# Optimization experiments

Hardware: AMD Instinct MI355X
Metric: run time of the kernel (lower is better)

The kernel has to match this reference:

```python
import jax, jax.numpy as jnp
import numpy as np

EPS = 1e-5


def _gcn_conv(x, src, dst, n_nodes, W, b):
    # x: [N, Fin]; src/dst: [E+N] (self-loops already appended)
    h = x @ W                                   # [N, Fout]
    deg = jnp.zeros((n_nodes,), x.dtype).at[dst].add(1.0)
    dinv = jax.lax.rsqrt(deg)                   # deg >= 1 due to self-loops
    norm = dinv[src] * dinv[dst]                # [E+N]
    msg = h[src] * norm[:, None]                # [E+N, Fout]  (gather)
    out = jax.ops.segment_sum(msg, dst, num_segments=n_nodes)  # scatter-add
    return out + b


def _bn_relu(x, gamma, beta):
    # BatchNorm over nodes (training-style batch statistics), then ReLU.
    mu = jnp.mean(x, axis=0)
    var = jnp.mean((x - mu) ** 2, axis=0)       # biased variance (torch BN)
    xn = (x - mu) * jax.lax.rsqrt(var + EPS)
    return jax.nn.relu(xn * gamma + beta)


def setup_inputs() -> dict:
    key = jax.random.key(0)
    ks = jax.random.split(key, 12)
    N, E, Fin, H, O, G = 100000, 1600000, 128, 128, 64, 128
    x = jax.random.normal(ks[0], (N, Fin), dtype=jnp.float32)
    edge_index = jax.random.randint(ks[1], (2, E), 0, N, dtype=jnp.int64)
    batch = jnp.sort(jax.random.randint(ks[2], (N,), 0, G, dtype=jnp.int64))
    s = 1.0 / np.sqrt(Fin)
    W0 = jax.random.uniform(ks[3], (Fin, H), jnp.float32, -s, s)
    b0 = jnp.zeros((H,), jnp.float32)
    g0 = jnp.ones((H,), jnp.float32)
    be0 = jnp.zeros((H,), jnp.float32)
    s2 = 1.0 / np.sqrt(H)
    W1 = jax.random.uniform(ks[4], (H, H), jnp.float32, -s2, s2)
    b1 = jnp.zeros((H,), jnp.float32)
    g1 = jnp.ones((H,), jnp.float32)
    be1 = jnp.zeros((H,), jnp.float32)
    Wout = jax.random.uniform(ks[5], (H, O), jnp.float32, -s2, s2)
    bout = jax.random.uniform(ks[6], (O,), jnp.float32, -s2, s2)
    return {"x": x, "edge_index": edge_index, "batch": batch, "num_graphs": 128,
            "W0": W0, "b0": b0, "g0": g0, "be0": be0,
            "W1": W1, "b1": b1, "g1": g1, "be1": be1,
            "Wout": Wout, "bout": bout}


def reference(x, edge_index, batch, num_graphs,
              W0, b0, g0, be0, W1, b1, g1, be1, Wout, bout):
    N = x.shape[0]
    loops = jnp.arange(N, dtype=edge_index.dtype)
    src = jnp.concatenate([edge_index[0], loops])  # add self-loops
    dst = jnp.concatenate([edge_index[1], loops])
    h = _gcn_conv(x, src, dst, N, W0, b0)
    h = _bn_relu(h, g0, be0)                       # Dropout(p=0.1) = identity in eval
    h = _gcn_conv(h, src, dst, N, W1, b1)
    h = _bn_relu(h, g1, be1)
    # global mean pool over graphs
    sums = jax.ops.segment_sum(h, batch, num_segments=num_graphs)   # [G, H]
    cnt = jax.ops.segment_sum(jnp.ones((N,), h.dtype), batch, num_segments=num_graphs)
    pooled = sums / jnp.maximum(cnt, 1.0)[:, None]
    return pooled @ Wout + bout
```

## Files before the change

kernel.cpp:

```cpp
#include <hip/hip_runtime.h>
#include <hip/hip_bf16.h>

typedef _Float16 half8_t __attribute__((ext_vector_type(8)));
typedef _Float16 half4_t __attribute__((ext_vector_type(4)));
typedef _Float16 half2_t __attribute__((ext_vector_type(2)));
typedef float float4_t __attribute__((ext_vector_type(4)));
typedef float float2_t __attribute__((ext_vector_type(2)));


__global__ __launch_bounds__(256) void k_hist(const int* __restrict__ dst, int E, int SH,
                                              int NBK, int WG, int CH, int* __restrict__ M) {
    extern __shared__ int lh[];
    for (int i = threadIdx.x; i < NBK; i += 256) lh[i] = 0;
    __syncthreads();
    int wg = blockIdx.x;
    int e0 = wg * CH, e1 = min(E, e0 + CH);
    for (int e = e0 + threadIdx.x; e < e1; e += 256)
        atomicAdd(&lh[dst[e] >> SH], 1);
    __syncthreads();
    for (int i = threadIdx.x; i < NBK; i += 256) M[i * WG + wg] = lh[i];
}

__global__ __launch_bounds__(256) void k_colscan(int* __restrict__ M, int WG,
                                                 int* __restrict__ totals) {
    __shared__ int s[256];
    int b = blockIdx.x, t = threadIdx.x;
    int v = (t < WG) ? M[b * WG + t] : 0;
    s[t] = v;
    __syncthreads();
    for (int off = 1; off < 256; off <<= 1) {
        int u = (t >= off) ? s[t - off] : 0;
        __syncthreads();
        s[t] += u;
        __syncthreads();
    }
    if (t < WG) M[b * WG + t] = s[t] - v;
    if (t == 255) totals[b] = s[255];
}

__global__ __launch_bounds__(512) void k_bucketscan(const int* __restrict__ totals, int NBK,
                                                    int E, int* __restrict__ base) {
    __shared__ int s[512];
    int t = threadIdx.x;
    int v = (t < NBK) ? totals[t] : 0;
    s[t] = v;
    __syncthreads();
    for (int off = 1; off < 512; off <<= 1) {
        int u = (t >= off) ? s[t - off] : 0;
        __syncthreads();
        s[t] += u;
        __syncthreads();
    }
    if (t < NBK) base[t] = s[t] - v;
    if (t == 0) base[NBK] = E;
}

__global__ __launch_bounds__(256) void k_scatter(const int* __restrict__ src,
                                                 const int* __restrict__ dst, int E, int SH,
                                                 int NBK, int WG, int CH,
                                                 const int* __restrict__ M,
                                                 const int* __restrict__ base,
                                                 unsigned* __restrict__ ebuf,
                                                 int* __restrict__ slots, int N) {
    if (slots) {
        int4 f; f.x = N; f.y = N; f.z = N; f.w = N;
        int total4 = N * 8;
        for (int idx = blockIdx.x * 256 + threadIdx.x; idx < total4; idx += gridDim.x * 256)
            ((int4*)slots)[idx] = f;
    }
    extern __shared__ int cur[];
    int wg = blockIdx.x;
    for (int i = threadIdx.x; i < NBK; i += 256) cur[i] = base[i] + M[i * WG + wg];
    __syncthreads();
    int e0 = wg * CH, e1 = min(E, e0 + CH);
    for (int e = e0 + threadIdx.x; e < e1; e += 256) {
        int d = dst[e];
        int b = d >> SH;
        int pos = atomicAdd(&cur[b], 1);
        ebuf[pos] = (unsigned)src[e] | ((unsigned)(d - (b << SH)) << 23);
    }
}

__global__ __launch_bounds__(256) void k_cntfill(const unsigned* __restrict__ ebuf,
                                                 const int* __restrict__ base, int SH, int N,
                                                 int E, float* __restrict__ dinv,
                                                 int* __restrict__ rp, int* __restrict__ colx,
                                                 int* __restrict__ slots,
                                                 const float* __restrict__ W0,
                                                 const float* __restrict__ W1,
                                                 _Float16* __restrict__ Wt0,
                                                 _Float16* __restrict__ Wt1,
                                                 const int* __restrict__ batch, int G,
                                                 int* __restrict__ gptr,
                                                 float* __restrict__ psum,
                                                 float* __restrict__ sums,
                                                 unsigned char* __restrict__ A8) {
    __shared__ int h[512];
    __shared__ int cur[512];
    __shared__ int rs[512];
    __shared__ int lim[512];
    __shared__ int s[256];
    int b = blockIdx.x, t = threadIdx.x;

    if (b < 64) {
        int idx = b * 256 + t;
        int n = idx >> 7, k = idx & 127;
        Wt0[n * 128 + k] = (_Float16)W0[k * 128 + n];
        Wt1[n * 128 + k] = (_Float16)W1[k * 128 + n];
    } else if (b == 64) {
        if (t <= G) {
            int g = t;
            int lo = 0, hi = N;
            while (lo < hi) {
                int mid = (lo + hi) >> 1;
                if (batch[mid] < g) lo = mid + 1; else hi = mid;
            }
            gptr[g] = lo;
        }
    } else if (b < 97) {
        int i0 = (b - 65) * 512 + t;
        psum[i0] = 0.f;
        psum[i0 + 256] = 0.f;
    } else if (b == 97) {
        if (t < 256) { sums[t] = 0.f; sums[t + 256] = 0.f; }
        if (t < 32) ((unsigned*)A8)[(size_t)N * 32 + t] = 0u;
    }

    int n0 = b << SH;
    int nb = min(N - n0, 1 << SH);
    for (int i = t; i < nb; i += 256) h[i] = 0;
    __syncthreads();
    int e0 = base[b], e1 = base[b + 1];
    for (int e = e0 + t; e < e1; e += 256)
        atomicAdd(&h[ebuf[e] >> 23], 1);
    __syncthreads();
    int i0 = 2 * t, i1 = 2 * t + 1;
    int a0 = (i0 < nb) ? h[i0] : 0;
    int a1 = (i1 < nb) ? h[i1] : 0;
    int ps = a0 + a1;
    s[t] = ps;
    __syncthreads();
    for (int off = 1; off < 256; off <<= 1) {
        int u = (t >= off) ? s[t - off] : 0;
        __syncthreads();
        s[t] += u;
        __syncthreads();
    }
    int excl = s[t] - ps;
    if (i0 < nb) {
        int r0 = e0 + excl;
        cur[i0] = r0;
        rs[i0] = r0;
        lim[i0] = min(a0, 32);
        rp[n0 + i0] = r0;
        dinv[n0 + i0] = rsqrtf((float)(a0 + 1));
    }
    if (i1 < nb) {
        int r1 = e0 + excl + a0;
        cur[i1] = r1;
        rs[i1] = r1;
        lim[i1] = min(a1, 32);
        rp[n0 + i1] = r1;
        dinv[n0 + i1] = rsqrtf((float)(a1 + 1));
    }
    if (b == (int)gridDim.x - 1 && t == 0) rp[N] = E;
    __syncthreads();
    for (int e = e0 + t; e < e1; e += 256) {
        unsigned v = ebuf[e];
        int local = (int)(v >> 23);
        int srcn = (int)(v & 0x7FFFFFu);
        int pos = atomicAdd(&cur[local], 1);
        colx[pos] = srcn;
        if (slots) {
            int off = pos - rs[local];
            if (off < lim[local]) {
                int idx = ((off & 3) << 3) + (off >> 2);
                slots[(size_t)(n0 + local) * 32 + idx] = srcn;
            }
        }
    }
}


__global__ __launch_bounds__(256) void k_gemmM(const float* __restrict__ X,
                                               const _Float16* __restrict__ Wt,
                                               const float* __restrict__ dinv,
                                               unsigned char* __restrict__ out, int N) {
    int t = threadIdx.x;
    int wv = t >> 6, lane = t & 63;
    int m = lane & 15, quad = lane >> 4;
    int rowbase = blockIdx.x * 64 + wv * 16;
    int arow = rowbase + m;
    int arowc = (arow < N) ? arow : (N - 1);
    const float* xr = X + (size_t)arowc * 128;

    float4_t acc[8];
    #pragma unroll
    for (int i = 0; i < 8; i++) acc[i] = (float4_t){0.f, 0.f, 0.f, 0.f};

    #pragma unroll
    for (int kc = 0; kc < 4; kc++) {
        int k0 = kc * 32 + quad * 8;
        float4 xa = *(const float4*)(xr + k0);
        float4 xb = *(const float4*)(xr + k0 + 4);
        float xv[8] = {xa.x, xa.y, xa.z, xa.w, xb.x, xb.y, xb.z, xb.w};
        half8_t a;
        #pragma unroll
        for (int j = 0; j < 8; j++) a[j] = (_Float16)xv[j];
        #pragma unroll
        for (int nt = 0; nt < 8; nt++) {
            half8_t b = *(const half8_t*)(Wt + (size_t)(nt * 16 + m) * 128 + k0);
            acc[nt] = __builtin_amdgcn_mfma_f32_16x16x32_f16(a, b, acc[nt], 0, 0, 0);
        }
    }

    float dv[4];
    #pragma unroll
    for (int r = 0; r < 4; r++) {
        int row = rowbase + quad * 4 + r;
        dv[r] = dinv[(row < N) ? row : (N - 1)];
    }
    #pragma unroll
    for (int r = 0; r < 4; r++) {
        int row = rowbase + quad * 4 + r;
        if (row < N) {
            unsigned char* o = out + (size_t)row * 128 + m;
            #pragma unroll
            for (int nt = 0; nt < 8; nt++) {
                float v = acc[nt][r] * dv[r];
                int pk = __builtin_amdgcn_cvt_pk_fp8_f32(v, v, 0, false);
                o[nt * 16] = (unsigned char)(pk & 0xFF);
            }
        }
    }
}

__global__ __launch_bounds__(256) void k_gemmM16(const _Float16* __restrict__ X,
                                                 const _Float16* __restrict__ Wt,
                                                 const float* __restrict__ sums,
                                                 const float* __restrict__ g,
                                                 const float* __restrict__ be,
                                                 const float* __restrict__ dinv,
                                                 unsigned char* __restrict__ out, int N) {
    __shared__ alignas(16) float ss[128];
    __shared__ alignas(16) float hh[128];
    int t = threadIdx.x;
    if (t < 128) {
        float invN = 1.0f / (float)N;
        float mu = sums[t] * invN;
        float var = fmaxf(sums[128 + t] * invN - mu * mu, 0.f);
        float sc = g[t] * rsqrtf(var + 1e-5f);
        ss[t] = sc;
        hh[t] = fmaf(-mu, sc, be[t]);
    }
    __syncthreads();

    int wv = t >> 6, lane = t & 63;
    int m = lane & 15, quad = lane >> 4;
    int rowbase = blockIdx.x * 64 + wv * 16;
    int arow = rowbase + m;
    int arowc = (arow < N) ? arow : (N - 1);
    const _Float16* xr = X + (size_t)arowc * 128;

    float4_t acc[8];
    #pragma unroll
    for (int i = 0; i < 8; i++) acc[i] = (float4_t){0.f, 0.f, 0.f, 0.f};

    #pragma unroll
    for (int kc = 0; kc < 4; kc++) {
        int k0 = kc * 32 + quad * 8;
        half8_t x8 = *(const half8_t*)(xr + k0);
        float4 sa = *(const float4*)(ss + k0);
        float4 sb = *(const float4*)(ss + k0 + 4);
        float4 ha = *(const float4*)(hh + k0);
        float4 hb = *(const float4*)(hh + k0 + 4);
        float sv[8] = {sa.x, sa.y, sa.z, sa.w, sb.x, sb.y, sb.z, sb.w};
        float hv[8] = {ha.x, ha.y, ha.z, ha.w, hb.x, hb.y, hb.z, hb.w};
        half8_t a;
        #pragma unroll
        for (int j = 0; j < 8; j++)
            a[j] = (_Float16)fmaxf(fmaf((float)x8[j], sv[j], hv[j]), 0.f);
        #pragma unroll
        for (int nt = 0; nt < 8; nt++) {
            half8_t b = *(const half8_t*)(Wt + (size_t)(nt * 16 + m) * 128 + k0);
            acc[nt] = __builtin_amdgcn_mfma_f32_16x16x32_f16(a, b, acc[nt], 0, 0, 0);
        }
    }

    float dv[4];
    #pragma unroll
    for (int r = 0; r < 4; r++) {
        int row = rowbase + quad * 4 + r;
        dv[r] = dinv[(row < N) ? row : (N - 1)];
    }
    #pragma unroll
    for (int r = 0; r < 4; r++) {
        int row = rowbase + quad * 4 + r;
        if (row < N) {
            unsigned char* o = out + (size_t)row * 128 + m;
            #pragma unroll
            for (int nt = 0; nt < 8; nt++) {
                float v = acc[nt][r] * dv[r];
                int pk = __builtin_amdgcn_cvt_pk_fp8_f32(v, v, 0, false);
                o[nt * 16] = (unsigned char)(pk & 0xFF);
            }
        }
    }
}


__device__ __forceinline__ void acc8(uint2 v, float2_t* a2) {
    a2[0] += __builtin_amdgcn_cvt_pk_f32_fp8((int)v.x, false);
    a2[1] += __builtin_amdgcn_cvt_pk_f32_fp8((int)v.x, true);
    a2[2] += __builtin_amdgcn_cvt_pk_f32_fp8((int)v.y, false);
    a2[3] += __builtin_amdgcn_cvt_pk_f32_fp8((int)v.y, true);
}

__device__ __forceinline__ void f8x4(unsigned w, float* o) {
    o[0] = __builtin_amdgcn_cvt_f32_fp8((int)w, 0);
    o[1] = __builtin_amdgcn_cvt_f32_fp8((int)w, 1);
    o[2] = __builtin_amdgcn_cvt_f32_fp8((int)w, 2);
    o[3] = __builtin_amdgcn_cvt_f32_fp8((int)w, 3);
}

__global__ __launch_bounds__(256) void k_aggS8(const unsigned char* __restrict__ hs,
                                               const int* __restrict__ slots,
                                               const int* __restrict__ rp,
                                               const int* __restrict__ colx,
                                               const float* __restrict__ dinv,
                                               const float* __restrict__ bias,
                                               _Float16* __restrict__ out, int N) {
    int wave = (blockIdx.x * 256 + threadIdx.x) >> 6;
    int lane = threadIdx.x & 63;
    if (wave >= N) return;
    int i = wave;
    int q = lane >> 4;
    int c8 = lane & 15;

    const int4* sl4 = (const int4*)(slots + (size_t)i * 32 + 8 * q);
    int4 sa = sl4[0];
    int k0 = rp[i], k1 = rp[i + 1];
    uint2 sw = *(const uint2*)(hs + (size_t)i * 128 + c8 * 8);
    int deg = k1 - k0;

    float2_t a2[4] = {{0.f, 0.f}, {0.f, 0.f}, {0.f, 0.f}, {0.f, 0.f}};

    {
        int ja[4] = {sa.x, sa.y, sa.z, sa.w};
        uint2 v[4];
        #pragma unroll
        for (int s = 0; s < 4; s++)
            v[s] = *(const uint2*)(hs + (size_t)ja[s] * 128 + c8 * 8);
        #pragma unroll
        for (int s = 0; s < 4; s++) acc8(v[s], a2);
    }
    if (deg > 16) {
        int4 sb = sl4[1];
        int jb[4] = {sb.x, sb.y, sb.z, sb.w};
        uint2 v[4];
        #pragma unroll
        for (int s = 0; s < 4; s++)
            v[s] = *(const uint2*)(hs + (size_t)jb[s] * 128 + c8 * 8);
        #pragma unroll
        for (int s = 0; s < 4; s++) acc8(v[s], a2);
        if (deg > 32) {
            for (int k = k0 + 32 + q; k < k1; k += 4) {
                uint2 vv = *(const uint2*)(hs + (size_t)colx[k] * 128 + c8 * 8);
                acc8(vv, a2);
            }
        }
    }

    float a[8] = {a2[0].x, a2[0].y, a2[1].x, a2[1].y,
                  a2[2].x, a2[2].y, a2[3].x, a2[3].y};
    #pragma unroll
    for (int t = 0; t < 8; t++) {
        float x = a[t];
        x += __shfl_xor(x, 16);
        x += __shfl_xor(x, 32);
        a[t] = x;
    }

    if (q == 0) {
        float d = dinv[i];
        float4 bA = ((const float4*)bias)[2 * c8];
        float4 bB = ((const float4*)bias)[2 * c8 + 1];
        float bb[8] = {bA.x, bA.y, bA.z, bA.w, bB.x, bB.y, bB.z, bB.w};
        float sf[8];
        f8x4(sw.x, sf);
        f8x4(sw.y, sf + 4);
        half8_t o;
        #pragma unroll
        for (int t = 0; t < 8; t++)
            o[t] = (_Float16)fmaf(a[t] + sf[t], d, bb[t]);
        ((half8_t*)out)[(size_t)i * 16 + c8] = o;
    }
}

__global__ __launch_bounds__(256) void k_aggC8(const unsigned char* __restrict__ hs,
                                               const int* __restrict__ rp,
                                               const int* __restrict__ colx,
                                               const float* __restrict__ dinv,
                                               const float* __restrict__ bias,
                                               _Float16* __restrict__ out, int N) {
    int wave = (blockIdx.x * 256 + threadIdx.x) >> 6;
    int lane = threadIdx.x & 63;
    if (wave >= N) return;
    int i = wave;
    int q = lane >> 4;
    int c8 = lane & 15;

    uint2 sw = *(const uint2*)(hs + (size_t)i * 128 + c8 * 8);
    int k0 = rp[i], k1 = rp[i + 1];

    float2_t a2[4] = {{0.f, 0.f}, {0.f, 0.f}, {0.f, 0.f}, {0.f, 0.f}};
    for (int k = k0 + q; k < k1; k += 4) {
        uint2 vv = *(const uint2*)(hs + (size_t)colx[k] * 128 + c8 * 8);
        acc8(vv, a2);
    }

    float a[8] = {a2[0].x, a2[0].y, a2[1].x, a2[1].y,
                  a2[2].x, a2[2].y, a2[3].x, a2[3].y};
    #pragma unroll
    for (int t = 0; t < 8; t++) {
        float x = a[t];
        x += __shfl_xor(x, 16);
        x += __shfl_xor(x, 32);
        a[t] = x;
    }

    if (q == 0) {
        float d = dinv[i];
        float4 bA = ((const float4*)bias)[2 * c8];
        float4 bB = ((const float4*)bias)[2 * c8 + 1];
        float bb[8] = {bA.x, bA.y, bA.z, bA.w, bB.x, bB.y, bB.z, bB.w};
        float sf[8];
        f8x4(sw.x, sf);
        f8x4(sw.y, sf + 4);
        half8_t o;
        #pragma unroll
        for (int t = 0; t < 8; t++)
            o[t] = (_Float16)fmaf(a[t] + sf[t], d, bb[t]);
        ((half8_t*)out)[(size_t)i * 16 + c8] = o;
    }
}


__global__ __launch_bounds__(256) void k_stats(const _Float16* __restrict__ x, int N,
                                               float* __restrict__ sums) {
    int lane = threadIdx.x & 63;
    int wv = threadIdx.x >> 6;
    int gw = blockIdx.x * 4 + wv;
    int stride = gridDim.x * 4;
    const half2_t* b = (const half2_t*)x;
    float2 s = make_float2(0.f, 0.f), q = make_float2(0.f, 0.f);
    for (int i = gw; i < N; i += stride) {
        half2_t v = b[(size_t)i * 64 + lane];
        float vx = (float)v.x, vy = (float)v.y;
        s.x += vx; s.y += vy;
        q.x += vx * vx; q.y += vy * vy;
    }
    __shared__ float ls[4][128];
    __shared__ float lq[4][128];
    ls[wv][2 * lane] = s.x; ls[wv][2 * lane + 1] = s.y;
    lq[wv][2 * lane] = q.x; lq[wv][2 * lane + 1] = q.y;
    __syncthreads();
    int t = threadIdx.x;
    if (t < 128) {
        float ts = ls[0][t] + ls[1][t] + ls[2][t] + ls[3][t];
        float tq = lq[0][t] + lq[1][t] + lq[2][t] + lq[3][t];
        atomicAdd(&sums[t], ts);
        atomicAdd(&sums[128 + t], tq);
    }
}


__global__ __launch_bounds__(256) void k_pool2(const _Float16* __restrict__ x,
                                               const int* __restrict__ batch,
                                               const float* __restrict__ sums,
                                               const float* __restrict__ g2,
                                               const float* __restrict__ be2,
                                               float* __restrict__ psum, int N) {
    __shared__ alignas(8) float ss[128];
    __shared__ alignas(8) float hh[128];
    int t = threadIdx.x;
    if (t < 128) {
        float invN = 1.0f / (float)N;
        float mu = sums[t] * invN;
        float var = fmaxf(sums[128 + t] * invN - mu * mu, 0.f);
        float sc = g2[t] * rsqrtf(var + 1e-5f);
        ss[t] = sc;
        hh[t] = fmaf(-mu, sc, be2[t]);
    }
    __syncthreads();

    int nw = gridDim.x * 4;
    int w = blockIdx.x * 4 + (threadIdx.x >> 6);
    int lane = threadIdx.x & 63;
    int per = (N + nw - 1) / nw;
    int i0 = w * per, i1 = min(N, i0 + per);
    if (i0 >= i1) return;
    const half2_t* b = (const half2_t*)x;
    float2 s2 = ((const float2*)ss)[lane];
    float2 h2 = ((const float2*)hh)[lane];
    float2 acc = make_float2(0.f, 0.f);
    int g = batch[i0];
    for (int i = i0; i < i1; i++) {
        int gi = batch[i];
        if (gi != g) {
            atomicAdd(&psum[g * 128 + 2 * lane], acc.x);
            atomicAdd(&psum[g * 128 + 2 * lane + 1], acc.y);
            acc = make_float2(0.f, 0.f);
            g = gi;
        }
        half2_t v = b[(size_t)i * 64 + lane];
        acc.x += fmaxf(fmaf((float)v.x, s2.x, h2.x), 0.f);
        acc.y += fmaxf(fmaf((float)v.y, s2.y, h2.y), 0.f);
    }
    atomicAdd(&psum[g * 128 + 2 * lane], acc.x);
    atomicAdd(&psum[g * 128 + 2 * lane + 1], acc.y);
}


__global__ __launch_bounds__(64) void k_final(const float* __restrict__ psum,
                                              const int* __restrict__ gptr,
                                              const float* __restrict__ Wout,
                                              const float* __restrict__ bout,
                                              float* __restrict__ out, int O) {
    int g = blockIdx.x, o = threadIdx.x;
    int cnt = gptr[g + 1] - gptr[g];
    float inv = 1.0f / fmaxf((float)cnt, 1.f);
    float acc = 0.f;
    for (int c = 0; c < 128; c++) acc = fmaf(psum[g * 128 + c], Wout[c * O + o], acc);
    out[g * O + o] = fmaf(acc, inv, bout[o]);
}


extern "C" void kernel_launch(void* const* d_in, const int* in_sizes, int n_in,
                              void* d_out, int out_size, void* d_ws, size_t ws_size,
                              hipStream_t stream) {
    const float* x    = (const float*)d_in[0];
    const int*   edge = (const int*)d_in[1];
    const int*   batch= (const int*)d_in[2];
    const float* W0   = (const float*)d_in[4];
    const float* b0   = (const float*)d_in[5];
    const float* g0   = (const float*)d_in[6];
    const float* be0  = (const float*)d_in[7];
    const float* W1   = (const float*)d_in[8];
    const float* b1   = (const float*)d_in[9];
    const float* g1   = (const float*)d_in[10];
    const float* be1  = (const float*)d_in[11];
    const float* Wout = (const float*)d_in[12];
    const float* bout = (const float*)d_in[13];
    float* out = (float*)d_out;

    const int Hh  = in_sizes[5];
    const int Fin = in_sizes[4] / Hh;
    const int N   = in_sizes[0] / Fin;
    const int E   = in_sizes[1] / 2;
    const int O   = in_sizes[13];
    const int G   = out_size / O;
    (void)Hh; (void)n_in;

    int SH = 8;
    while (((N + (1 << SH) - 1) >> SH) > 512) SH++;
    const int NBK = (N + (1 << SH) - 1) >> SH;
    const int CH  = ((E + 255) / 256 > 8192) ? (E + 255) / 256 : 8192;
    const int WG  = (E + CH - 1) / CH;

    char* p = (char*)d_ws;
    auto alloc = [&](size_t bytes) -> void* {
        void* r = (void*)p;
        p += (bytes + 255) & ~(size_t)255;
        return r;
    };
    unsigned char* A8 = (unsigned char*)alloc((size_t)(N + 1) * 128);
    _Float16* B   = (_Float16*)alloc((size_t)(N + 1) * 128 * 2);
    float* dinv   = (float*)alloc((size_t)N * 4);
    int*   rp     = (int*)alloc((size_t)(N + 1) * 4);
    int*   colx   = (int*)alloc((size_t)E * 4);
    unsigned* ebuf= (unsigned*)alloc((size_t)E * 4);
    int*   M      = (int*)alloc((size_t)NBK * WG * 4);
    int*   totals = (int*)alloc((size_t)NBK * 4);
    int*   base   = (int*)alloc((size_t)(NBK + 1) * 4);
    float* sums   = (float*)alloc(512 * 4);
    int*   gptr   = (int*)alloc((size_t)(G + 1) * 4);
    float* psum   = (float*)alloc((size_t)G * 128 * 4);
    _Float16* Wt0 = (_Float16*)alloc(128 * 128 * 2);
    _Float16* Wt1 = (_Float16*)alloc(128 * 128 * 2);
    int*   slots  = (int*)alloc((size_t)N * 32 * 4);
    bool useSlots = ((size_t)(p - (char*)d_ws) <= ws_size);
    if (!useSlots) slots = nullptr;

    const int* src = edge;
    const int* dst = edge + E;

    k_hist<<<WG, 256, NBK * 4, stream>>>(dst, E, SH, NBK, WG, CH, M);
    k_colscan<<<NBK, 256, 0, stream>>>(M, WG, totals);
    k_bucketscan<<<1, 512, 0, stream>>>(totals, NBK, E, base);
    k_scatter<<<WG, 256, NBK * 4, stream>>>(src, dst, E, SH, NBK, WG, CH, M, base, ebuf,
                                            slots, N);
    k_cntfill<<<NBK, 256, 0, stream>>>(ebuf, base, SH, N, E, dinv, rp, colx, slots,
                                       W0, W1, Wt0, Wt1, batch, G, gptr, psum, sums, A8);

    k_gemmM<<<(N + 63) / 64, 256, 0, stream>>>(x, Wt0, dinv, A8, N);
    if (useSlots)
        k_aggS8<<<(N + 3) / 4, 256, 0, stream>>>(A8, slots, rp, colx, dinv, b0, B, N);
    else
        k_aggC8<<<(N + 3) / 4, 256, 0, stream>>>(A8, rp, colx, dinv, b0, B, N);
    k_stats<<<512, 256, 0, stream>>>(B, N, sums);

    k_gemmM16<<<(N + 63) / 64, 256, 0, stream>>>(B, Wt1, sums, g0, be0, dinv, A8, N);
    if (useSlots)
        k_aggS8<<<(N + 3) / 4, 256, 0, stream>>>(A8, slots, rp, colx, dinv, b1, B, N);
    else
        k_aggC8<<<(N + 3) / 4, 256, 0, stream>>>(A8, rp, colx, dinv, b1, B, N);
    k_stats<<<512, 256, 0, stream>>>(B, N, sums + 256);

    k_pool2<<<512, 256, 0, stream>>>(B, batch, sums + 256, g1, be1, psum, N);
    k_final<<<G, 64, 0, stream>>>(psum, gptr, Wout, bout, out, O);
}
```

Before: 401.6 us.

## Replace CSR build with atomic per-node slot scatter and overflow list

Removes the five-kernel bucketed CSR construction (histogram, two scans, bucket scatter, count/fill). Each edge now claims a position in its destination's 32-entry slot row with one global atomic on a per-node counter; edges beyond 32 go to a small global overflow list. Degree normalisation is recomputed from the counter instead of a stored dinv, and unused slots are masked by degree rather than pre-filled. The trade-offs: slot order becomes nondeterministic, high-degree nodes must scan the entire overflow list, and edges past OVFCAP are silently dropped.

Result: slower. 476.6 us (+18.7%).

```diff
diff --git a/kernel.cpp b/kernel.cpp
--- a/kernel.cpp
+++ b/kernel.cpp
@@ -2,106 +2,25 @@
 #include <hip/hip_bf16.h>
 
 typedef _Float16 half8_t __attribute__((ext_vector_type(8)));
-typedef _Float16 half4_t __attribute__((ext_vector_type(4)));
 typedef _Float16 half2_t __attribute__((ext_vector_type(2)));
 typedef float float4_t __attribute__((ext_vector_type(4)));
 typedef float float2_t __attribute__((ext_vector_type(2)));
 
-
-__global__ __launch_bounds__(256) void k_hist(const int* __restrict__ dst, int E, int SH,
-                                              int NBK, int WG, int CH, int* __restrict__ M) {
-    extern __shared__ int lh[];
-    for (int i = threadIdx.x; i < NBK; i += 256) lh[i] = 0;
-    __syncthreads();
-    int wg = blockIdx.x;
-    int e0 = wg * CH, e1 = min(E, e0 + CH);
-    for (int e = e0 + threadIdx.x; e < e1; e += 256)
-        atomicAdd(&lh[dst[e] >> SH], 1);
-    __syncthreads();
-    for (int i = threadIdx.x; i < NBK; i += 256) M[i * WG + wg] = lh[i];
-}
-
-__global__ __launch_bounds__(256) void k_colscan(int* __restrict__ M, int WG,
-                                                 int* __restrict__ totals) {
-    __shared__ int s[256];
+#define OVFCAP 65536
+
+
+__global__ __launch_bounds__(256) void k_prep(const float* __restrict__ W0,
+                                              const float* __restrict__ W1,
+                                              _Float16* __restrict__ Wt0,
+                                              _Float16* __restrict__ Wt1,
+                                              const int* __restrict__ batch, int G,
+                                              int* __restrict__ gptr,
+                                              float* __restrict__ psum,
+                                              float* __restrict__ sums,
+                                              unsigned char* __restrict__ A8,
+                                              int* __restrict__ cnt,
+                                              int* __restrict__ ovfcnt, int N) {
     int b = blockIdx.x, t = threadIdx.x;
-    int v = (t < WG) ? M[b * WG + t] : 0;
-    s[t] = v;
-    __syncthreads();
-    for (int off = 1; off < 256; off <<= 1) {
-        int u = (t >= off) ? s[t - off] : 0;
-        __syncthreads();
-        s[t] += u;
-        __syncthreads();
-    }
-    if (t < WG) M[b * WG + t] = s[t] - v;
-    if (t == 255) totals[b] = s[255];
-}
-
-__global__ __launch_bounds__(512) void k_bucketscan(const int* __restrict__ totals, int NBK,
-                                                    int E, int* __restrict__ base) {
-    __shared__ int s[512];
-    int t = threadIdx.x;
-    int v = (t < NBK) ? totals[t] : 0;
-    s[t] = v;
-    __syncthreads();
-    for (int off = 1; off < 512; off <<= 1) {
-        int u = (t >= off) ? s[t - off] : 0;
-        __syncthreads();
-        s[t] += u;
-        __syncthreads();
-    }
-    if (t < NBK) base[t] = s[t] - v;
-    if (t == 0) base[NBK] = E;
-}
-
-__global__ __launch_bounds__(256) void k_scatter(const int* __restrict__ src,
-                                                 const int* __restrict__ dst, int E, int SH,
-                                                 int NBK, int WG, int CH,
-                                                 const int* __restrict__ M,
-                                                 const int* __restrict__ base,
-                                                 unsigned* __restrict__ ebuf,
-                                                 int* __restrict__ slots, int N) {
-    if (slots) {
-        int4 f; f.x = N; f.y = N; f.z = N; f.w = N;
-        int total4 = N * 8;
-        for (int idx = blockIdx.x * 256 + threadIdx.x; idx < total4; idx += gridDim.x * 256)
-            ((int4*)slots)[idx] = f;
-    }
-    extern __shared__ int cur[];
-    int wg = blockIdx.x;
-    for (int i = threadIdx.x; i < NBK; i += 256) cur[i] = base[i] + M[i * WG + wg];
-    __syncthreads();
-    int e0 = wg * CH, e1 = min(E, e0 + CH);
-    for (int e = e0 + threadIdx.x; e < e1; e += 256) {
-        int d = dst[e];
-        int b = d >> SH;
-        int pos = atomicAdd(&cur[b], 1);
-        ebuf[pos] = (unsigned)src[e] | ((unsigned)(d - (b << SH)) << 23);
-    }
-}
-
-__global__ __launch_bounds__(256) void k_cntfill(const unsigned* __restrict__ ebuf,
-                                                 const int* __restrict__ base, int SH, int N,
-                                                 int E, float* __restrict__ dinv,
-                                                 int* __restrict__ rp, int* __restrict__ colx,
-                                                 int* __restrict__ slots,
-                                                 const float* __restrict__ W0,
-                                                 const float* __restrict__ W1,
-                                                 _Float16* __restrict__ Wt0,
-                                                 _Float16* __restrict__ Wt1,
-                                                 const int* __restrict__ batch, int G,
-                                                 int* __restrict__ gptr,
-                                                 float* __restrict__ psum,
-                                                 float* __restrict__ sums,
-                                                 unsigned char* __restrict__ A8) {
-    __shared__ int h[512];
-    __shared__ int cur[512];
-    __shared__ int rs[512];
-    __shared__ int lim[512];
-    __shared__ int s[256];
-    int b = blockIdx.x, t = threadIdx.x;
-
     if (b < 64) {
         int idx = b * 256 + t;
         int n = idx >> 7, k = idx & 127;
@@ -124,59 +43,27 @@
     } else if (b == 97) {
         if (t < 256) { sums[t] = 0.f; sums[t + 256] = 0.f; }
         if (t < 32) ((unsigned*)A8)[(size_t)N * 32 + t] = 0u;
-    }
-
-    int n0 = b << SH;
-    int nb = min(N - n0, 1 << SH);
-    for (int i = t; i < nb; i += 256) h[i] = 0;
-    __syncthreads();
-    int e0 = base[b], e1 = base[b + 1];
-    for (int e = e0 + t; e < e1; e += 256)
-        atomicAdd(&h[ebuf[e] >> 23], 1);
-    __syncthreads();
-    int i0 = 2 * t, i1 = 2 * t + 1;
-    int a0 = (i0 < nb) ? h[i0] : 0;
-    int a1 = (i1 < nb) ? h[i1] : 0;
-    int ps = a0 + a1;
-    s[t] = ps;
-    __syncthreads();
-    for (int off = 1; off < 256; off <<= 1) {
-        int u = (t >= off) ? s[t - off] : 0;
-        __syncthreads();
-        s[t] += u;
-        __syncthreads();
-    }
-    int excl = s[t] - ps;
-    if (i0 < nb) {
-        int r0 = e0 + excl;
-        cur[i0] = r0;
-        rs[i0] = r0;
-        lim[i0] = min(a0, 32);
-        rp[n0 + i0] = r0;
-        dinv[n0 + i0] = rsqrtf((float)(a0 + 1));
-    }
-    if (i1 < nb) {
-        int r1 = e0 + excl + a0;
-        cur[i1] = r1;
-        rs[i1] = r1;
-        lim[i1] = min(a1, 32);
-        rp[n0 + i1] = r1;
-        dinv[n0 + i1] = rsqrtf((float)(a1 + 1));
-    }
-    if (b == (int)gridDim.x - 1 && t == 0) rp[N] = E;
-    __syncthreads();
-    for (int e = e0 + t; e < e1; e += 256) {
-        unsigned v = ebuf[e];
-        int local = (int)(v >> 23);
-        int srcn = (int)(v & 0x7FFFFFu);
-        int pos = atomicAdd(&cur[local], 1);
-        colx[pos] = srcn;
-        if (slots) {
-            int off = pos - rs[local];
-            if (off < lim[local]) {
-                int idx = ((off & 3) << 3) + (off >> 2);
-                slots[(size_t)(n0 + local) * 32 + idx] = srcn;
-            }
+        if (t == 255) *ovfcnt = 0;
+    }
+    for (int i = b * 256 + t; i < N; i += gridDim.x * 256) cnt[i] = 0;
+}
+
+
+__global__ __launch_bounds__(256) void k_slotscatter(const int* __restrict__ src,
+                                                     const int* __restrict__ dst, int E,
+                                                     int* __restrict__ cnt,
+                                                     int* __restrict__ slots,
+                                                     int2* __restrict__ ovf,
+                                                     int* __restrict__ ovfcnt) {
+    int stride = gridDim.x * 256;
+    for (int e = blockIdx.x * 256 + threadIdx.x; e < E; e += stride) {
+        int d = dst[e], s = src[e];
+        int pos = atomicAdd(&cnt[d], 1);
+        if (pos < 32) {
+            slots[(size_t)d * 32 + ((pos & 3) << 3) + (pos >> 2)] = s;
+        } else {
+            int o = atomicAdd(ovfcnt, 1);
+            if (o < OVFCAP) ovf[o] = make_int2(d, s);
         }
     }
 }
@@ -184,7 +71,7 @@
 
 __global__ __launch_bounds__(256) void k_gemmM(const float* __restrict__ X,
                                                const _Float16* __restrict__ Wt,
-                                               const float* __restrict__ dinv,
+                                               const int* __restrict__ cnt,
                                                unsigned char* __restrict__ out, int N) {
     int t = threadIdx.x;
     int wv = t >> 6, lane = t & 63;
@@ -218,7 +105,7 @@
     #pragma unroll
     for (int r = 0; r < 4; r++) {
         int row = rowbase + quad * 4 + r;
-        dv[r] = dinv[(row < N) ? row : (N - 1)];
+        dv[r] = rsqrtf((float)(cnt[(row < N) ? row : (N - 1)] + 1));
     }
     #pragma unroll
     for (int r = 0; r < 4; r++) {
@@ -240,7 +127,7 @@
                                                  const float* __restrict__ sums,
                                                  const float* __restrict__ g,
                                                  const float* __restrict__ be,
-                                                 const float* __restrict__ dinv,
+                                                 const int* __restrict__ cnt,
                                                  unsigned char* __restrict__ out, int N) {
     __shared__ alignas(16) float ss[128];
     __shared__ alignas(16) float hh[128];
@@ -291,7 +178,7 @@
     #pragma unroll
     for (int r = 0; r < 4; r++) {
         int row = rowbase + quad * 4 + r;
-        dv[r] = dinv[(row < N) ? row : (N - 1)];
+        dv[r] = rsqrtf((float)(cnt[(row < N) ? row : (N - 1)] + 1));
     }
     #pragma unroll
     for (int r = 0; r < 4; r++) {
@@ -325,9 +212,9 @@
 
 __global__ __launch_bounds__(256) void k_aggS8(const unsigned char* __restrict__ hs,
                                                const int* __restrict__ slots,
-                                               const int* __restrict__ rp,
-                                               const int* __restrict__ colx,
-                                               const float* __restrict__ dinv,
+                                               const int* __restrict__ cnt,
+                                               const int2* __restrict__ ovf,
+                                               const int* __restrict__ ovfcnt,
                                                const float* __restrict__ bias,
                                                _Float16* __restrict__ out, int N) {
     int wave = (blockIdx.x * 256 + threadIdx.x) >> 6;
@@ -339,34 +226,45 @@
 
     const int4* sl4 = (const int4*)(slots + (size_t)i * 32 + 8 * q);
     int4 sa = sl4[0];
-    int k0 = rp[i], k1 = rp[i + 1];
+    int deg = cnt[i];
     uint2 sw = *(const uint2*)(hs + (size_t)i * 128 + c8 * 8);
-    int deg = k1 - k0;
 
     float2_t a2[4] = {{0.f, 0.f}, {0.f, 0.f}, {0.f, 0.f}, {0.f, 0.f}};
 
     {
-        int ja[4] = {sa.x, sa.y, sa.z, sa.w};
+        int jraw[4] = {sa.x, sa.y, sa.z, sa.w};
+        int j[4];
+        #pragma unroll
+        for (int s = 0; s < 4; s++)
+            j[s] = (q + 4 * s < deg) ? jraw[s] : N;
         uint2 v[4];
         #pragma unroll
         for (int s = 0; s < 4; s++)
-            v[s] = *(const uint2*)(hs + (size_t)ja[s] * 128 + c8 * 8);
+            v[s] = *(const uint2*)(hs + (size_t)j[s] * 128 + c8 * 8);
         #pragma unroll
         for (int s = 0; s < 4; s++) acc8(v[s], a2);
     }
     if (deg > 16) {
         int4 sb = sl4[1];
-        int jb[4] = {sb.x, sb.y, sb.z, sb.w};
+        int jraw[4] = {sb.x, sb.y, sb.z, sb.w};
+        int j[4];
+        #pragma unroll
+        for (int s = 0; s < 4; s++)
+            j[s] = (16 + q + 4 * s < deg) ? jraw[s] : N;
         uint2 v[4];
         #pragma unroll
         for (int s = 0; s < 4; s++)
-            v[s] = *(const uint2*)(hs + (size_t)jb[s] * 128 + c8 * 8);
+            v[s] = *(const uint2*)(hs + (size_t)j[s] * 128 + c8 * 8);
         #pragma unroll
         for (int s = 0; s < 4; s++) acc8(v[s], a2);
         if (deg > 32) {
-            for (int k = k0 + 32 + q; k < k1; k += 4) {
-                uint2 vv = *(const uint2*)(hs + (size_t)colx[k] * 128 + c8 * 8);
-                acc8(vv, a2);
+            int oc = min(*ovfcnt, OVFCAP);
+            for (int k = 0; k < oc; k++) {
+                int2 pr = ovf[k];
+                if (pr.x == i && (k & 3) == q) {
+                    uint2 vv = *(const uint2*)(hs + (size_t)pr.y * 128 + c8 * 8);
+                    acc8(vv, a2);
+                }
             }
         }
     }
@@ -382,55 +280,7 @@
     }
 
     if (q == 0) {
-        float d = dinv[i];
-        float4 bA = ((const float4*)bias)[2 * c8];
-        float4 bB = ((const float4*)bias)[2 * c8 + 1];
-        float bb[8] = {bA.x, bA.y, bA.z, bA.w, bB.x, bB.y, bB.z, bB.w};
-        float sf[8];
-        f8x4(sw.x, sf);
-        f8x4(sw.y, sf + 4);
-        half8_t o;
-        #pragma unroll
-        for (int t = 0; t < 8; t++)
-            o[t] = (_Float16)fmaf(a[t] + sf[t], d, bb[t]);
-        ((half8_t*)out)[(size_t)i * 16 + c8] = o;
-    }
-}
-
-__global__ __launch_bounds__(256) void k_aggC8(const unsigned char* __restrict__ hs,
-                                               const int* __restrict__ rp,
-                                               const int* __restrict__ colx,
-                                               const float* __restrict__ dinv,
-                                               const float* __restrict__ bias,
-                                               _Float16* __restrict__ out, int N) {
-    int wave = (blockIdx.x * 256 + threadIdx.x) >> 6;
-    int lane = threadIdx.x & 63;
-    if (wave >= N) return;
-    int i = wave;
-    int q = lane >> 4;
-    int c8 = lane & 15;
-
-    uint2 sw = *(const uint2*)(hs + (size_t)i * 128 + c8 * 8);
-    int k0 = rp[i], k1 = rp[i + 1];
-
-    float2_t a2[4] = {{0.f, 0.f}, {0.f, 0.f}, {0.f, 0.f}, {0.f, 0.f}};
-    for (int k = k0 + q; k < k1; k += 4) {
-        uint2 vv = *(const uint2*)(hs + (size_t)colx[k] * 128 + c8 * 8);
-        acc8(vv, a2);
-    }
-
-    float a[8] = {a2[0].x, a2[0].y, a2[1].x, a2[1].y,
-                  a2[2].x, a2[2].y, a2[3].x, a2[3].y};
-    #pragma unroll
-    for (int t = 0; t < 8; t++) {
-        float x = a[t];
-        x += __shfl_xor(x, 16);
-        x += __shfl_xor(x, 32);
-        a[t] = x;
-    }
-
-    if (q == 0) {
-        float d = dinv[i];
+        float d = rsqrtf((float)(deg + 1));
         float4 bA = ((const float4*)bias)[2 * c8];
         float4 bB = ((const float4*)bias)[2 * c8 + 1];
         float bb[8] = {bA.x, bA.y, bA.z, bA.w, bB.x, bB.y, bB.z, bB.w};
@@ -560,13 +410,7 @@
     const int E   = in_sizes[1] / 2;
     const int O   = in_sizes[13];
     const int G   = out_size / O;
-    (void)Hh; (void)n_in;
-
-    int SH = 8;
-    while (((N + (1 << SH) - 1) >> SH) > 512) SH++;
-    const int NBK = (N + (1 << SH) - 1) >> SH;
-    const int CH  = ((E + 255) / 256 > 8192) ? (E + 255) / 256 : 8192;
-    const int WG  = (E + CH - 1) / CH;
+    (void)Hh; (void)n_in; (void)ws_size;
 
     char* p = (char*)d_ws;
     auto alloc = [&](size_t bytes) -> void* {
@@ -575,46 +419,30 @@
         return r;
     };
     unsigned char* A8 = (unsigned char*)alloc((size_t)(N + 1) * 128);
-    _Float16* B   = (_Float16*)alloc((size_t)(N + 1) * 128 * 2);
-    float* dinv   = (float*)alloc((size_t)N * 4);
-    int*   rp     = (int*)alloc((size_t)(N + 1) * 4);
-    int*   colx   = (int*)alloc((size_t)E * 4);
-    unsigned* ebuf= (unsigned*)alloc((size_t)E * 4);
-    int*   M      = (int*)alloc((size_t)NBK * WG * 4);
-    int*   totals = (int*)alloc((size_t)NBK * 4);
-    int*   base   = (int*)alloc((size_t)(NBK + 1) * 4);
+    _Float16* B   = (_Float16*)alloc((size_t)N * 128 * 2);
+    int*   cnt    = (int*)alloc((size_t)N * 4);
+    int*   slots  = (int*)alloc((size_t)N * 32 * 4);
+    int2*  ovf    = (int2*)alloc((size_t)OVFCAP * 8);
+    int*   ovfcnt = (int*)alloc(256);
     float* sums   = (float*)alloc(512 * 4);
     int*   gptr   = (int*)alloc((size_t)(G + 1) * 4);
     float* psum   = (float*)alloc((size_t)G * 128 * 4);
     _Float16* Wt0 = (_Float16*)alloc(128 * 128 * 2);
     _Float16* Wt1 = (_Float16*)alloc(128 * 128 * 2);
-    int*   slots  = (int*)alloc((size_t)N * 32 * 4);
-    bool useSlots = ((size_t)(p - (char*)d_ws) <= ws_size);
-    if (!useSlots) slots = nullptr;
 
     const int* src = edge;
     const int* dst = edge + E;
 
-    k_hist<<<WG, 256, NBK * 4, stream>>>(dst, E, SH, NBK, WG, CH, M);
-    k_colscan<<<NBK, 256, 0, stream>>>(M, WG, totals);
-    k_bucketscan<<<1, 512, 0, stream>>>(totals, NBK, E, base);
-    k_scatter<<<WG, 256, NBK * 4, stream>>>(src, dst, E, SH, NBK, WG, CH, M, base, ebuf,
-                                            slots, N);
-    k_cntfill<<<NBK, 256, 0, stream>>>(ebuf, base, SH, N, E, dinv, rp, colx, slots,
-                                       W0, W1, Wt0, Wt1, batch, G, gptr, psum, sums, A8);
-
-    k_gemmM<<<(N + 63) / 64, 256, 0, stream>>>(x, Wt0, dinv, A8, N);
-    if (useSlots)
-        k_aggS8<<<(N + 3) / 4, 256, 0, stream>>>(A8, slots, rp, colx, dinv, b0, B, N);
-    else
-        k_aggC8<<<(N + 3) / 4, 256, 0, stream>>>(A8, rp, colx, dinv, b0, B, N);
+    k_prep<<<128, 256, 0, stream>>>(W0, W1, Wt0, Wt1, batch, G, gptr, psum, sums,
+                                    A8, cnt, ovfcnt, N);
+    k_slotscatter<<<2048, 256, 0, stream>>>(src, dst, E, cnt, slots, ovf, ovfcnt);
+
+    k_gemmM<<<(N + 63) / 64, 256, 0, stream>>>(x, Wt0, cnt, A8, N);
+    k_aggS8<<<(N + 3) / 4, 256, 0, stream>>>(A8, slots, cnt, ovf, ovfcnt, b0, B, N);
     k_stats<<<512, 256, 0, stream>>>(B, N, sums);
 
-    k_gemmM16<<<(N + 63) / 64, 256, 0, stream>>>(B, Wt1, sums, g0, be0, dinv, A8, N);
-    if (useSlots)
-        k_aggS8<<<(N + 3) / 4, 256, 0, stream>>>(A8, slots, rp, colx, dinv, b1, B, N);
-    else
-        k_aggC8<<<(N + 3) / 4, 256, 0, stream>>>(A8, rp, colx, dinv, b1, B, N);
+    k_gemmM16<<<(N + 63) / 64, 256, 0, stream>>>(B, Wt1, sums, g0, be0, cnt, A8, N);
+    k_aggS8<<<(N + 3) / 4, 256, 0, stream>>>(A8, slots, cnt, ovf, ovfcnt, b1, B, N);
     k_stats<<<512, 256, 0, stream>>>(B, N, sums + 256);
 
     k_pool2<<<512, 256, 0, stream>>>(B, batch, sums + 256, g1, be1, psum, N);
```

## Drop slot prefill, mask padded slots, skip redundant colx writes, recompute dinv

Applied to the files above, without the earlier changes.

The scatter kernel no longer fills the whole slots table with the sentinel N. Instead, the aggregation kernel masks slot indices at or beyond the node degree so they point to the padding row. The fill kernel now writes each edge either to its slot or to colx, not both, which cuts global write traffic during CSR build. The aggregation kernels recompute dinv from the degree instead of loading it, and the GEMM input loads use nontemporal hints. The main risk is correctness: aggS8 must read colx only for edges past the slot limit, and padding row N of A8 must be zero.

After: 400.4 us. Within noise of the previous version (-0.3%).

```diff
diff --git a/kernel.cpp b/kernel.cpp
--- a/kernel.cpp
+++ b/kernel.cpp
@@ -2,10 +2,10 @@
 #include <hip/hip_bf16.h>
 
 typedef _Float16 half8_t __attribute__((ext_vector_type(8)));
-typedef _Float16 half4_t __attribute__((ext_vector_type(4)));
 typedef _Float16 half2_t __attribute__((ext_vector_type(2)));
 typedef float float4_t __attribute__((ext_vector_type(4)));
 typedef float float2_t __attribute__((ext_vector_type(2)));
+typedef unsigned int uint4_t __attribute__((ext_vector_type(4)));
 
 
 __global__ __launch_bounds__(256) void k_hist(const int* __restrict__ dst, int E, int SH,
@@ -60,14 +60,7 @@
                                                  int NBK, int WG, int CH,
                                                  const int* __restrict__ M,
                                                  const int* __restrict__ base,
-                                                 unsigned* __restrict__ ebuf,
-                                                 int* __restrict__ slots, int N) {
-    if (slots) {
-        int4 f; f.x = N; f.y = N; f.z = N; f.w = N;
-        int total4 = N * 8;
-        for (int idx = blockIdx.x * 256 + threadIdx.x; idx < total4; idx += gridDim.x * 256)
-            ((int4*)slots)[idx] = f;
-    }
+                                                 unsigned* __restrict__ ebuf) {
     extern __shared__ int cur[];
     int wg = blockIdx.x;
     for (int i = threadIdx.x; i < NBK; i += 256) cur[i] = base[i] + M[i * WG + wg];
@@ -170,13 +163,12 @@
         int local = (int)(v >> 23);
         int srcn = (int)(v & 0x7FFFFFu);
         int pos = atomicAdd(&cur[local], 1);
-        colx[pos] = srcn;
-        if (slots) {
-            int off = pos - rs[local];
-            if (off < lim[local]) {
-                int idx = ((off & 3) << 3) + (off >> 2);
-                slots[(size_t)(n0 + local) * 32 + idx] = srcn;
-            }
+        int off = pos - rs[local];
+        if (slots && off < lim[local]) {
+            int idx = ((off & 3) << 3) + (off >> 2);
+            slots[(size_t)(n0 + local) * 32 + idx] = srcn;
+        } else {
+            colx[pos] = srcn;
         }
     }
 }
@@ -201,12 +193,13 @@
     #pragma unroll
     for (int kc = 0; kc < 4; kc++) {
         int k0 = kc * 32 + quad * 8;
-        float4 xa = *(const float4*)(xr + k0);
-        float4 xb = *(const float4*)(xr + k0 + 4);
-        float xv[8] = {xa.x, xa.y, xa.z, xa.w, xb.x, xb.y, xb.z, xb.w};
+        float4_t xa = __builtin_nontemporal_load((const float4_t*)(xr + k0));
+        float4_t xb = __builtin_nontemporal_load((const float4_t*)(xr + k0 + 4));
         half8_t a;
         #pragma unroll
-        for (int j = 0; j < 8; j++) a[j] = (_Float16)xv[j];
+        for (int j = 0; j < 4; j++) a[j] = (_Float16)xa[j];
+        #pragma unroll
+        for (int j = 0; j < 4; j++) a[4 + j] = (_Float16)xb[j];
         #pragma unroll
         for (int nt = 0; nt < 8; nt++) {
             half8_t b = *(const half8_t*)(Wt + (size_t)(nt * 16 + m) * 128 + k0);
@@ -269,17 +262,19 @@
     #pragma unroll
     for (int kc = 0; kc < 4; kc++) {
         int k0 = kc * 32 + quad * 8;
-        half8_t x8 = *(const half8_t*)(xr + k0);
-        float4 sa = *(const float4*)(ss + k0);
-        float4 sb = *(const float4*)(ss + k0 + 4);
-        float4 ha = *(const float4*)(hh + k0);
-        float4 hb = *(const float4*)(hh + k0 + 4);
-        float sv[8] = {sa.x, sa.y, sa.z, sa.w, sb.x, sb.y, sb.z, sb.w};
-        float hv[8] = {ha.x, ha.y, ha.z, ha.w, hb.x, hb.y, hb.z, hb.w};
+        uint4_t xraw = __builtin_nontemporal_load((const uint4_t*)(xr + k0));
+        half8_t x8 = __builtin_bit_cast(half8_t, xraw);
+        float4_t sa = *(const float4_t*)(ss + k0);
+        float4_t sb = *(const float4_t*)(ss + k0 + 4);
+        float4_t ha = *(const float4_t*)(hh + k0);
+        float4_t hb = *(const float4_t*)(hh + k0 + 4);
         half8_t a;
         #pragma unroll
-        for (int j = 0; j < 8; j++)
-            a[j] = (_Float16)fmaxf(fmaf((float)x8[j], sv[j], hv[j]), 0.f);
+        for (int j = 0; j < 4; j++)
+            a[j] = (_Float16)fmaxf(fmaf((float)x8[j], sa[j], ha[j]), 0.f);
+        #pragma unroll
+        for (int j = 0; j < 4; j++)
+            a[4 + j] = (_Float16)fmaxf(fmaf((float)x8[4 + j], sb[j], hb[j]), 0.f);
         #pragma unroll
         for (int nt = 0; nt < 8; nt++) {
             half8_t b = *(const half8_t*)(Wt + (size_t)(nt * 16 + m) * 128 + k0);
@@ -327,7 +322,6 @@
                                                const int* __restrict__ slots,
                                                const int* __restrict__ rp,
                                                const int* __restrict__ colx,
-                                               const float* __restrict__ dinv,
                                                const float* __restrict__ bias,
                                                _Float16* __restrict__ out, int N) {
     int wave = (blockIdx.x * 256 + threadIdx.x) >> 6;
@@ -346,21 +340,29 @@
     float2_t a2[4] = {{0.f, 0.f}, {0.f, 0.f}, {0.f, 0.f}, {0.f, 0.f}};
 
     {
-        int ja[4] = {sa.x, sa.y, sa.z, sa.w};
+        int jraw[4] = {sa.x, sa.y, sa.z, sa.w};
+        int j[4];
+        #pragma unroll
+        for (int s = 0; s < 4; s++)
+            j[s] = (q + 4 * s < deg) ? jraw[s] : N;
         uint2 v[4];
         #pragma unroll
         for (int s = 0; s < 4; s++)
-            v[s] = *(const uint2*)(hs + (size_t)ja[s] * 128 + c8 * 8);
+            v[s] = *(const uint2*)(hs + (size_t)j[s] * 128 + c8 * 8);
         #pragma unroll
         for (int s = 0; s < 4; s++) acc8(v[s], a2);
     }
     if (deg > 16) {
         int4 sb = sl4[1];
-        int jb[4] = {sb.x, sb.y, sb.z, sb.w};
+        int jraw[4] = {sb.x, sb.y, sb.z, sb.w};
+        int j[4];
+        #pragma unroll
+        for (int s = 0; s < 4; s++)
+            j[s] = (16 + q + 4 * s < deg) ? jraw[s] : N;
         uint2 v[4];
         #pragma unroll
         for (int s = 0; s < 4; s++)
-            v[s] = *(const uint2*)(hs + (size_t)jb[s] * 128 + c8 * 8);
+            v[s] = *(const uint2*)(hs + (size_t)j[s] * 128 + c8 * 8);
         #pragma unroll
         for (int s = 0; s < 4; s++) acc8(v[s], a2);
         if (deg > 32) {
@@ -382,7 +384,7 @@
     }
 
     if (q == 0) {
-        float d = dinv[i];
+        float d = rsqrtf((float)(deg + 1));
         float4 bA = ((const float4*)bias)[2 * c8];
         float4 bB = ((const float4*)bias)[2 * c8 + 1];
         float bb[8] = {bA.x, bA.y, bA.z, bA.w, bB.x, bB.y, bB.z, bB.w};
@@ -400,7 +402,6 @@
 __global__ __launch_bounds__(256) void k_aggC8(const unsigned char* __restrict__ hs,
                                                const int* __restrict__ rp,
                                                const int* __restrict__ colx,
-                                               const float* __restrict__ dinv,
                                                const float* __restrict__ bias,
                                                _Float16* __restrict__ out, int N) {
     int wave = (blockIdx.x * 256 + threadIdx.x) >> 6;
@@ -430,7 +431,7 @@
     }
 
     if (q == 0) {
-        float d = dinv[i];
+        float d = rsqrtf((float)(k1 - k0 + 1));
         float4 bA = ((const float4*)bias)[2 * c8];
         float4 bB = ((const float4*)bias)[2 * c8 + 1];
         float bb[8] = {bA.x, bA.y, bA.z, bA.w, bB.x, bB.y, bB.z, bB.w};
@@ -575,7 +576,7 @@
         return r;
     };
     unsigned char* A8 = (unsigned char*)alloc((size_t)(N + 1) * 128);
-    _Float16* B   = (_Float16*)alloc((size_t)(N + 1) * 128 * 2);
+    _Float16* B   = (_Float16*)alloc((size_t)N * 128 * 2);
     float* dinv   = (float*)alloc((size_t)N * 4);
     int*   rp     = (int*)alloc((size_t)(N + 1) * 4);
     int*   colx   = (int*)alloc((size_t)E * 4);
@@ -598,23 +599,22 @@
     k_hist<<<WG, 256, NBK * 4, stream>>>(dst, E, SH, NBK, WG, CH, M);
     k_colscan<<<NBK, 256, 0, stream>>>(M, WG, totals);
     k_bucketscan<<<1, 512, 0, stream>>>(totals, NBK, E, base);
-    k_scatter<<<WG, 256, NBK * 4, stream>>>(src, dst, E, SH, NBK, WG, CH, M, base, ebuf,
-                                            slots, N);
+    k_scatter<<<WG, 256, NBK * 4, stream>>>(src, dst, E, SH, NBK, WG, CH, M, base, ebuf);
     k_cntfill<<<NBK, 256, 0, stream>>>(ebuf, base, SH, N, E, dinv, rp, colx, slots,
                                        W0, W1, Wt0, Wt1, batch, G, gptr, psum, sums, A8);
 
     k_gemmM<<<(N + 63) / 64, 256, 0, stream>>>(x, Wt0, dinv, A8, N);
     if (useSlots)
-        k_aggS8<<<(N + 3) / 4, 256, 0, stream>>>(A8, slots, rp, colx, dinv, b0, B, N);
+        k_aggS8<<<(N + 3) / 4, 256, 0, stream>>>(A8, slots, rp, colx, b0, B, N);
     else
-        k_aggC8<<<(N + 3) / 4, 256, 0, stream>>>(A8, rp, colx, dinv, b0, B, N);
+        k_aggC8<<<(N + 3) / 4, 256, 0, stream>>>(A8, rp, colx, b0, B, N);
     k_stats<<<512, 256, 0, stream>>>(B, N, sums);
 
     k_gemmM16<<<(N + 63) / 64, 256, 0, stream>>>(B, Wt1, sums, g0, be0, dinv, A8, N);
     if (useSlots)
-        k_aggS8<<<(N + 3) / 4, 256, 0, stream>>>(A8, slots, rp, colx, dinv, b1, B, N);
+        k_aggS8<<<(N + 3) / 4, 256, 0, stream>>>(A8, slots, rp, colx, b1, B, N);
     else
-        k_aggC8<<<(N + 3) / 4, 256, 0, stream>>>(A8, rp, colx, dinv, b1, B, N);
+        k_aggC8<<<(N + 3) / 4, 256, 0, stream>>>(A8, rp, colx, b1, B, N);
     k_stats<<<512, 256, 0, stream>>>(B, N, sums + 256);
 
     k_pool2<<<512, 256, 0, stream>>>(B, batch, sums + 256, g1, be1, psum, N);
```
